# Kernel tuning notes

Hardware: AMD Instinct MI355X
Metric: run time of the kernel (lower is better)

## Reference

```python
import jax, jax.numpy as jnp
import numpy as np

B, N = 128, 2048
QUERY_DIM, NODE_DIM, OUT_DIM = 256, 128, 256
LAMBDA_INIT = 0.8
LN_EPS = 1e-5


def setup_inputs() -> dict:
    key = jax.random.key(0)
    ks = jax.random.split(key, 8)
    fp_vec = jax.random.normal(ks[0], (B, QUERY_DIM), dtype=jnp.float32)
    node_mat = jax.random.normal(ks[1], (B, N, NODE_DIM), dtype=jnp.float32)
    mask = jax.random.uniform(ks[2], (B, N)) < 0.75
    s = 1.0 / np.sqrt(QUERY_DIM)
    Wq1 = jax.random.uniform(ks[3], (NODE_DIM, QUERY_DIM), minval=-s, maxval=s, dtype=jnp.float32)
    Wq2 = jax.random.uniform(ks[4], (NODE_DIM, QUERY_DIM), minval=-s, maxval=s, dtype=jnp.float32)
    s2 = 1.0 / np.sqrt(NODE_DIM)
    Wk = jax.random.uniform(ks[5], (NODE_DIM, NODE_DIM), minval=-s2, maxval=s2, dtype=jnp.float32)
    Wv = jax.random.uniform(ks[6], (OUT_DIM, NODE_DIM), minval=-s2, maxval=s2, dtype=jnp.float32)
    lambda_logit = jnp.zeros((1,), dtype=jnp.float32)
    gamma = jnp.ones((OUT_DIM,), dtype=jnp.float32)
    beta = jnp.zeros((OUT_DIM,), dtype=jnp.float32)
    return {"fp_vec": fp_vec, "node_mat": node_mat, "mask": mask,
            "Wq1": Wq1, "Wq2": Wq2, "Wk": Wk, "Wv": Wv,
            "lambda_logit": lambda_logit, "gamma": gamma, "beta": beta}


def reference(fp_vec, node_mat, mask, Wq1, Wq2, Wk, Wv, lambda_logit, gamma, beta):
    node_dim = node_mat.shape[-1]
    inv_scale = 1.0 / jnp.sqrt(jnp.asarray(node_dim, jnp.float32))
    # projections (torch Linear: y = x @ W.T)
    q1 = fp_vec @ Wq1.T            # (B, node_dim)
    q2 = fp_vec @ Wq2.T            # (B, node_dim)
    k = jnp.einsum('bnd,ed->bne', node_mat, Wk)   # (B, N, node_dim)
    v = jnp.einsum('bnd,od->bno', node_mat, Wv)   # (B, N, out_dim)
    # single-query scores over nodes
    s1 = jnp.einsum('bd,bnd->bn', q1, k) * inv_scale
    s2 = jnp.einsum('bd,bnd->bn', q2, k) * inv_scale
    pad = jnp.where(mask, 0.0, -1e9).astype(s1.dtype)  # (B, N)
    A1 = jax.nn.softmax(s1 + pad, axis=-1)
    A2 = jax.nn.softmax(s2 + pad, axis=-1)
    lam = LAMBDA_INIT + jax.nn.sigmoid(lambda_logit) * 0.2  # (1,)
    A_diff = A1 - lam * A2         # dropout inactive (eval)
    z = jnp.einsum('bn,bno->bo', A_diff, v)  # (B, out_dim)
    # LayerNorm
    mu = jnp.mean(z, axis=-1, keepdims=True)
    var = jnp.mean(jnp.square(z - mu), axis=-1, keepdims=True)
    return (z - mu) * jax.lax.rsqrt(var + LN_EPS) * gamma + beta
```

## Files before the change

### kernel.cpp

```cpp
#include <hip/hip_runtime.h>
#include <hip/hip_bf16.h>
#include <math.h>

#define BB 128
#define NN 2048
#define ND 128
#define QD 256
#define OD 256
#define CHUNKS 32
#define ROWS_PER_CHUNK (NN / CHUNKS)
#define PART_STRIDE 260

#define EXP2F(x) __builtin_amdgcn_exp2f(x)

typedef __attribute__((address_space(1))) const void gvoid_t;
typedef __attribute__((address_space(3))) void lvoid_t;

__global__ __launch_bounds__(128) void proj_kernel(
    const float* __restrict__ fp_vec, const float* __restrict__ Wq1,
    const float* __restrict__ Wq2, const float* __restrict__ Wk,
    float* __restrict__ qk1g, float* __restrict__ qk2g)
{
  __shared__ __align__(16) float fp_s[QD];
  __shared__ float q1_s[ND];
  __shared__ float q2_s[ND];
  const int b = blockIdx.x, t = threadIdx.x;
  fp_s[t]       = fp_vec[b * QD + t];
  fp_s[t + 128] = fp_vec[b * QD + 128 + t];
  __syncthreads();
  float a1 = 0.f, a2 = 0.f;
  const float4* w1p = (const float4*)(Wq1 + t * QD);
  const float4* w2p = (const float4*)(Wq2 + t * QD);
  #pragma unroll 8
  for (int q = 0; q < QD / 4; ++q) {
    float4 wa = w1p[q], wb = w2p[q];
    float4 f = *(const float4*)&fp_s[q * 4];
    a1 += f.x * wa.x + f.y * wa.y + f.z * wa.z + f.w * wa.w;
    a2 += f.x * wb.x + f.y * wb.y + f.z * wb.z + f.w * wb.w;
  }
  q1_s[t] = a1;
  q2_s[t] = a2;
  __syncthreads();
  float k1 = 0.f, k2 = 0.f;
  #pragma unroll 8
  for (int e = 0; e < ND; ++e) {
    float wv = Wk[e * ND + t];
    k1 += q1_s[e] * wv;
    k2 += q2_s[e] * wv;
  }
  const float cscale = 0.08838834764831845f * 1.4426950408889634f;
  qk1g[b * ND + t] = k1 * cscale;
  qk2g[b * ND + t] = k2 * cscale;
}

__global__ __launch_bounds__(256) void attn_kernel(
    const float* __restrict__ node, const int* __restrict__ mask,
    const float* __restrict__ qk1g, const float* __restrict__ qk2g,
    float* __restrict__ part)
{
  const int bid = blockIdx.x;
  const int b = bid >> 5;
  const int c = bid & (CHUNKS - 1);
  const int t = threadIdx.x;
  const int wave = t >> 6;
  const int lane = t & 63;
  const int half = lane >> 5;
  const int hl = lane & 31;

  __shared__ __align__(16) float tile_s[ROWS_PER_CHUNK * ND];
  __shared__ float pad_s[ROWS_PER_CHUNK];
  __shared__ float sl1[4], sl2[4];
  __shared__ __align__(16) float sw1[4][ND], sw2[4][ND];

  const int chunk_row0 = c * ROWS_PER_CHUNK;
  if (t < ROWS_PER_CHUNK)
    pad_s[t] = mask[b * NN + chunk_row0 + t] ? 0.f : -1e9f;

  {
    const char* gb = (const char*)(node + (size_t)b * NN * ND
                                   + (size_t)chunk_row0 * ND);
    const char* gw = gb + wave * 8192 + lane * 16;
    char* lw = ((char*)tile_s) + wave * 8192;
    #pragma unroll
    for (int i = 0; i < 8; ++i) {
      __builtin_amdgcn_global_load_lds(
          (gvoid_t*)(gw + i * 1024),
          (lvoid_t*)(lw + i * 1024),
          16, 0, 0);
    }
  }

  const float4 qk1 = *(const float4*)(qk1g + b * ND + hl * 4);
  const float4 qk2 = *(const float4*)(qk2g + b * ND + hl * 4);

  __syncthreads();

  float l1 = 0.f, l2 = 0.f;
  float4 w1 = make_float4(0.f, 0.f, 0.f, 0.f);
  float4 w2 = make_float4(0.f, 0.f, 0.f, 0.f);

  #pragma unroll
  for (int j = 0; j < 8; ++j) {
    const int r = 16 * wave + 2 * j + half;
    const float4 x = *(const float4*)&tile_s[r * ND + hl * 4];
    const float pad = pad_s[r];

    float d1 = x.x * qk1.x + x.y * qk1.y + x.z * qk1.z + x.w * qk1.w;
    float d2 = x.x * qk2.x + x.y * qk2.y + x.z * qk2.z + x.w * qk2.w;
    #pragma unroll
    for (int off = 1; off < 32; off <<= 1) {
      d1 += __shfl_xor(d1, off, 64);
      d2 += __shfl_xor(d2, off, 64);
    }
    const float p1 = EXP2F(d1 + pad);
    const float p2 = EXP2F(d2 + pad);
    l1 += p1;
    l2 += p2;
    w1.x += p1 * x.x; w1.y += p1 * x.y; w1.z += p1 * x.z; w1.w += p1 * x.w;
    w2.x += p2 * x.x; w2.y += p2 * x.y; w2.z += p2 * x.z; w2.w += p2 * x.w;
  }

  l1 += __shfl_xor(l1, 32, 64);
  l2 += __shfl_xor(l2, 32, 64);
  w1.x += __shfl_xor(w1.x, 32, 64); w1.y += __shfl_xor(w1.y, 32, 64);
  w1.z += __shfl_xor(w1.z, 32, 64); w1.w += __shfl_xor(w1.w, 32, 64);
  w2.x += __shfl_xor(w2.x, 32, 64); w2.y += __shfl_xor(w2.y, 32, 64);
  w2.z += __shfl_xor(w2.z, 32, 64); w2.w += __shfl_xor(w2.w, 32, 64);
  if (half == 0) {
    *(float4*)&sw1[wave][hl * 4] = w1;
    *(float4*)&sw2[wave][hl * 4] = w2;
    if (hl == 0) { sl1[wave] = l1; sl2[wave] = l2; }
  }
  __syncthreads();

  float* po = part + (size_t)bid * PART_STRIDE;
  if (t == 0) {
    po[0] = sl1[0] + sl1[1] + sl1[2] + sl1[3];
    po[1] = sl2[0] + sl2[1] + sl2[2] + sl2[3];
  }
  if (t < ND) {
    po[4 + t]   = sw1[0][t] + sw1[1][t] + sw1[2][t] + sw1[3][t];
    po[132 + t] = sw2[0][t] + sw2[1][t] + sw2[2][t] + sw2[3][t];
  }
}

__global__ __launch_bounds__(256) void finish_kernel(
    const float* __restrict__ part, const float* __restrict__ Wv,
    const float* __restrict__ lambda_logit, const float* __restrict__ gamma,
    const float* __restrict__ beta, float* __restrict__ out)
{
  const int b = blockIdx.x, t = threadIdx.x;
  __shared__ __align__(16) float wd_s[ND];
  __shared__ float red[8];

  const float lam = 0.8f + 0.2f / (1.f + __expf(-lambda_logit[0]));
  const float* pb = part + (size_t)b * CHUNKS * PART_STRIDE;

  if (t < ND) {
    float L1 = 0.f, L2 = 0.f, W1 = 0.f, W2 = 0.f;
    #pragma unroll 8
    for (int i = 0; i < CHUNKS; ++i) {
      const float* pc = pb + (size_t)i * PART_STRIDE;
      L1 += pc[0];
      L2 += pc[1];
      W1 += pc[4 + t];
      W2 += pc[132 + t];
    }
    wd_s[t] = W1 / L1 - lam * (W2 / L2);
  }
  __syncthreads();

  float z = 0.f;
  const float4* wvp = (const float4*)(Wv + t * ND);
  #pragma unroll 8
  for (int d = 0; d < ND / 4; ++d) {
    const float4 w = wvp[d];
    const float4 f = *(const float4*)&wd_s[d * 4];
    z += f.x * w.x + f.y * w.y + f.z * w.z + f.w * w.w;
  }

  const int wave = t >> 6, lane = t & 63;
  float s = z;
  #pragma unroll
  for (int off = 32; off; off >>= 1) s += __shfl_xor(s, off, 64);
  if (lane == 0) red[wave] = s;
  __syncthreads();
  const float mu = (red[0] + red[1] + red[2] + red[3]) * (1.f / OD);
  const float dz = z - mu;
  float vs = dz * dz;
  #pragma unroll
  for (int off = 32; off; off >>= 1) vs += __shfl_xor(vs, off, 64);
  if (lane == 0) red[wave + 4] = vs;
  __syncthreads();
  const float var = (red[4] + red[5] + red[6] + red[7]) * (1.f / OD);
  out[b * OD + t] = dz * rsqrtf(var + 1e-5f) * gamma[t] + beta[t];
}

extern "C" void kernel_launch(void* const* d_in, const int* in_sizes, int n_in,
                              void* d_out, int out_size, void* d_ws, size_t ws_size,
                              hipStream_t stream) {
  const float* fp_vec = (const float*)d_in[0];
  const float* node   = (const float*)d_in[1];
  const int*   mask   = (const int*)d_in[2];
  const float* Wq1    = (const float*)d_in[3];
  const float* Wq2    = (const float*)d_in[4];
  const float* Wk     = (const float*)d_in[5];
  const float* Wv     = (const float*)d_in[6];
  const float* ll     = (const float*)d_in[7];
  const float* gamma  = (const float*)d_in[8];
  const float* beta   = (const float*)d_in[9];
  float* out = (float*)d_out;

  float* qk1g = (float*)d_ws;
  float* qk2g = qk1g + BB * ND;
  float* part = qk2g + BB * ND;

  proj_kernel<<<BB, 128, 0, stream>>>(fp_vec, Wq1, Wq2, Wk, qk1g, qk2g);
  attn_kernel<<<BB * CHUNKS, 256, 0, stream>>>(node, mask, qk1g, qk2g, part);
  finish_kernel<<<BB, 256, 0, stream>>>(part, Wv, ll, gamma, beta, out);
}
```

Measured before the change: 238.2 us.

## Double-buffer per-wave node tiles with async LDS loads over fewer, longer blocks

Each block now covers 256 rows instead of 64, split into per-wave streams of 64 rows. Each wave prefetches 8-row steps into a private double buffer with global_load_lds and waits on vmcnt, so loads overlap compute instead of a single load-then-compute phase. The dot-product reduction packs both score sums into one shuffle chain, and the mask is read from a register via shuffle instead of LDS. This cuts the block count and the partial sums the finish kernel has to read. The cost is lower parallelism (1024 blocks), reliance on hand-written waitcnt ordering, and reduced occupancy headroom.

```diff
diff --git a/kernel.cpp b/kernel.cpp
--- a/kernel.cpp
+++ b/kernel.cpp
@@ -7,8 +7,13 @@
 #define ND 128
 #define QD 256
 #define OD 256
-#define CHUNKS 32
-#define ROWS_PER_CHUNK (NN / CHUNKS)
+
+#define NPART 8
+#define ROWS_PER_BLOCK (NN / NPART)
+#define ROWS_PER_WAVE  (ROWS_PER_BLOCK / 4)
+#define STEPS 8
+#define STEP_ROWS (ROWS_PER_WAVE / STEPS)
+#define STEP_BYTES (STEP_ROWS * ND * 4)
 #define PART_STRIDE 260
 
 #define EXP2F(x) __builtin_amdgcn_exp2f(x)
@@ -53,71 +58,94 @@
   qk2g[b * ND + t] = k2 * cscale;
 }
 
-__global__ __launch_bounds__(256) void attn_kernel(
+__global__ __launch_bounds__(256, 4) void attn_kernel(
     const float* __restrict__ node, const int* __restrict__ mask,
     const float* __restrict__ qk1g, const float* __restrict__ qk2g,
     float* __restrict__ part)
 {
   const int bid = blockIdx.x;
-  const int b = bid >> 5;
-  const int c = bid & (CHUNKS - 1);
+  const int b   = bid >> 3;
+  const int oct = bid & (NPART - 1);
   const int t = threadIdx.x;
-  const int wave = t >> 6;
+  const int w = t >> 6;
   const int lane = t & 63;
   const int half = lane >> 5;
   const int hl = lane & 31;
 
-  __shared__ __align__(16) float tile_s[ROWS_PER_CHUNK * ND];
-  __shared__ float pad_s[ROWS_PER_CHUNK];
+  __shared__ __align__(16) float tile_s[4][2][STEP_ROWS * ND];
+  __shared__ __align__(16) float sw1[4][ND], sw2[4][ND];
   __shared__ float sl1[4], sl2[4];
-  __shared__ __align__(16) float sw1[4][ND], sw2[4][ND];
-
-  const int chunk_row0 = c * ROWS_PER_CHUNK;
-  if (t < ROWS_PER_CHUNK)
-    pad_s[t] = mask[b * NN + chunk_row0 + t] ? 0.f : -1e9f;
-
-  {
-    const char* gb = (const char*)(node + (size_t)b * NN * ND
-                                   + (size_t)chunk_row0 * ND);
-    const char* gw = gb + wave * 8192 + lane * 16;
-    char* lw = ((char*)tile_s) + wave * 8192;
-    #pragma unroll
-    for (int i = 0; i < 8; ++i) {
-      __builtin_amdgcn_global_load_lds(
-          (gvoid_t*)(gw + i * 1024),
-          (lvoid_t*)(lw + i * 1024),
-          16, 0, 0);
-    }
-  }
+
+  const int wrow0 = oct * ROWS_PER_BLOCK + w * ROWS_PER_WAVE;
 
   const float4 qk1 = *(const float4*)(qk1g + b * ND + hl * 4);
   const float4 qk2 = *(const float4*)(qk2g + b * ND + hl * 4);
-
-  __syncthreads();
+  const int mv = mask[b * NN + wrow0 + lane];
+
+  const char* gbase = (const char*)node + (size_t)(b * NN + wrow0) * (ND * 4);
+  char* lb0 = (char*)&tile_s[w][0][0];
+  char* lb1 = (char*)&tile_s[w][1][0];
+
+  #pragma unroll
+  for (int i = 0; i < 4; ++i)
+    __builtin_amdgcn_global_load_lds(
+        (gvoid_t*)(gbase + lane * 16 + i * 1024),
+        (lvoid_t*)(lb0 + i * 1024), 16, 0, 0);
+  #pragma unroll
+  for (int i = 0; i < 4; ++i)
+    __builtin_amdgcn_global_load_lds(
+        (gvoid_t*)(gbase + STEP_BYTES + lane * 16 + i * 1024),
+        (lvoid_t*)(lb1 + i * 1024), 16, 0, 0);
+
+  const float pv = mv ? 0.f : -1e9f;
 
   float l1 = 0.f, l2 = 0.f;
   float4 w1 = make_float4(0.f, 0.f, 0.f, 0.f);
   float4 w2 = make_float4(0.f, 0.f, 0.f, 0.f);
 
-  #pragma unroll
-  for (int j = 0; j < 8; ++j) {
-    const int r = 16 * wave + 2 * j + half;
-    const float4 x = *(const float4*)&tile_s[r * ND + hl * 4];
-    const float pad = pad_s[r];
-
-    float d1 = x.x * qk1.x + x.y * qk1.y + x.z * qk1.z + x.w * qk1.w;
-    float d2 = x.x * qk2.x + x.y * qk2.y + x.z * qk2.z + x.w * qk2.w;
+  #pragma unroll 2
+  for (int s = 0; s < STEPS; ++s) {
+    if (s < STEPS - 1) asm volatile("s_waitcnt vmcnt(4)" ::: "memory");
+    else               asm volatile("s_waitcnt vmcnt(0)" ::: "memory");
+    __builtin_amdgcn_sched_barrier(0);
+
+    const float* buf = &tile_s[w][s & 1][0];
+    const int ib = s * STEP_ROWS;
+
     #pragma unroll
-    for (int off = 1; off < 32; off <<= 1) {
-      d1 += __shfl_xor(d1, off, 64);
-      d2 += __shfl_xor(d2, off, 64);
+    for (int j = 0; j < STEP_ROWS / 2; ++j) {
+      const float4 x = *(const float4*)&buf[(2 * j + half) * ND + hl * 4];
+      float d1 = x.x * qk1.x + x.y * qk1.y + x.z * qk1.z + x.w * qk1.w;
+      float d2 = x.x * qk2.x + x.y * qk2.y + x.z * qk2.z + x.w * qk2.w;
+      float e1 = d1 + __shfl_xor(d1, 1, 64);
+      float e2 = d2 + __shfl_xor(d2, 1, 64);
+      float m = (lane & 1) ? e2 : e1;
+      m += __shfl_xor(m, 2, 64);
+      m += __shfl_xor(m, 4, 64);
+      m += __shfl_xor(m, 8, 64);
+      m += __shfl_xor(m, 16, 64);
+      const float mo = __shfl_xor(m, 1, 64);
+      const float s1 = (lane & 1) ? mo : m;
+      const float s2 = (lane & 1) ? m : mo;
+      const float pad = __shfl(pv, ib + 2 * j + half, 64);
+      const float p1 = EXP2F(s1 + pad);
+      const float p2 = EXP2F(s2 + pad);
+      l1 += p1;
+      l2 += p2;
+      w1.x += p1 * x.x; w1.y += p1 * x.y; w1.z += p1 * x.z; w1.w += p1 * x.w;
+      w2.x += p2 * x.x; w2.y += p2 * x.y; w2.z += p2 * x.z; w2.w += p2 * x.w;
     }
-    const float p1 = EXP2F(d1 + pad);
-    const float p2 = EXP2F(d2 + pad);
-    l1 += p1;
-    l2 += p2;
-    w1.x += p1 * x.x; w1.y += p1 * x.y; w1.z += p1 * x.z; w1.w += p1 * x.w;
-    w2.x += p2 * x.x; w2.y += p2 * x.y; w2.z += p2 * x.z; w2.w += p2 * x.w;
+
+    asm volatile("s_waitcnt lgkmcnt(0)" ::: "memory");
+    if (s + 2 < STEPS) {
+      const char* gs = gbase + (size_t)(s + 2) * STEP_BYTES + lane * 16;
+      char* ls = (char*)&tile_s[w][s & 1][0];
+      #pragma unroll
+      for (int i = 0; i < 4; ++i)
+        __builtin_amdgcn_global_load_lds(
+            (gvoid_t*)(gs + i * 1024),
+            (lvoid_t*)(ls + i * 1024), 16, 0, 0);
+    }
   }
 
   l1 += __shfl_xor(l1, 32, 64);
@@ -127,9 +155,9 @@
   w2.x += __shfl_xor(w2.x, 32, 64); w2.y += __shfl_xor(w2.y, 32, 64);
   w2.z += __shfl_xor(w2.z, 32, 64); w2.w += __shfl_xor(w2.w, 32, 64);
   if (half == 0) {
-    *(float4*)&sw1[wave][hl * 4] = w1;
-    *(float4*)&sw2[wave][hl * 4] = w2;
-    if (hl == 0) { sl1[wave] = l1; sl2[wave] = l2; }
+    *(float4*)&sw1[w][hl * 4] = w1;
+    *(float4*)&sw2[w][hl * 4] = w2;
+    if (hl == 0) { sl1[w] = l1; sl2[w] = l2; }
   }
   __syncthreads();
 
@@ -154,12 +182,12 @@
   __shared__ float red[8];
 
   const float lam = 0.8f + 0.2f / (1.f + __expf(-lambda_logit[0]));
-  const float* pb = part + (size_t)b * CHUNKS * PART_STRIDE;
+  const float* pb = part + (size_t)b * NPART * PART_STRIDE;
 
   if (t < ND) {
     float L1 = 0.f, L2 = 0.f, W1 = 0.f, W2 = 0.f;
-    #pragma unroll 8
-    for (int i = 0; i < CHUNKS; ++i) {
+    #pragma unroll
+    for (int i = 0; i < NPART; ++i) {
       const float* pc = pb + (size_t)i * PART_STRIDE;
       L1 += pc[0];
       L2 += pc[1];
@@ -216,6 +244,6 @@
   float* part = qk2g + BB * ND;
 
   proj_kernel<<<BB, 128, 0, stream>>>(fp_vec, Wq1, Wq2, Wk, qk1g, qk2g);
-  attn_kernel<<<BB * CHUNKS, 256, 0, stream>>>(node, mask, qk1g, qk2g, part);
+  attn_kernel<<<BB * NPART, 256, 0, stream>>>(node, mask, qk1g, qk2g, part);
   finish_kernel<<<BB, 256, 0, stream>>>(part, Wv, ll, gamma, beta, out);
 }
```

After: 235.7 us. Within noise of the previous version (-1.0%).
